# Kernel optimization log

Hardware: AMD Instinct MI355X
Metric: run time of the kernel (lower is better)

The kernel has to match this reference:

```python
import jax, jax.numpy as jnp
import numpy as np
import math

B = 1024
G = 34  # grid_dim = 17*2
C = 4
SCENT = 19


def _scent_kernel_np():
    h = w = SCENT
    mx, my = 0.5 * h, 0.5 * w
    sx, sy = h / 4.0, w / 4.0
    x = np.linspace(0.0, h, h)
    y = np.linspace(0.0, w, w)
    X, Y = np.meshgrid(x, y, indexing='ij')
    z = (1.0 / (2.0 * math.pi * sx * sy)) * np.exp(-(((X - mx) ** 2) / (2 * sx ** 2) + ((Y - my) ** 2) / (2 * sy ** 2)))
    return (z * 80.0).astype(np.float32)


def setup_inputs() -> dict:
    key = jax.random.key(0)
    k1, k2, k3, k4 = jax.random.split(key, 4)
    cell = jax.random.uniform(k1, (B, C, G, G), dtype=jnp.float32)
    food = (jax.random.uniform(k2, (B, G, G), dtype=jnp.float32) > 0.97).astype(jnp.float32)
    fc1_w = jax.random.normal(k3, (64, 12), dtype=jnp.float32) * (1.0 / np.sqrt(12))
    fc1_b = jnp.zeros((64,), dtype=jnp.float32)
    fc2_w = jax.random.normal(k4, (4, 64), dtype=jnp.float32) * (1.0 / np.sqrt(64))
    fc2_b = jnp.zeros((4,), dtype=jnp.float32)
    scent_kernel = jnp.asarray(_scent_kernel_np())
    return {"cell": cell, "food": food, "fc1_w": fc1_w, "fc1_b": fc1_b,
            "fc2_w": fc2_w, "fc2_b": fc2_b, "scent_kernel": scent_kernel, "steps": 32}


def _conv(x, w, pad, groups):
    # x: [B, Cin, H, W], w: [Cout, Cin/groups, kh, kw]; cross-correlation like torch
    return jax.lax.conv_general_dilated(
        x, w, window_strides=(1, 1), padding=[(pad, pad), (pad, pad)],
        feature_group_count=groups, dimension_numbers=('NCHW', 'OIHW', 'NCHW'))


def _maxpool3(x):
    # 3x3 max pool, stride 1, pad 1 (pad value -inf, matching torch MaxPool2d semantics)
    return jax.lax.reduce_window(x, -jnp.inf, jax.lax.max, (1, 1, 3, 3), (1, 1, 1, 1),
                                 [(0, 0), (0, 0), (1, 1), (1, 1)])


def _forward(cell, food, fc1_w, fc1_b, fc2_w, fc2_b, scent_kernel, steps):
    dx = jnp.outer(jnp.array([1., 2., 1.], jnp.float32), jnp.array([-1., 0., 1.], jnp.float32)) / 8.0
    dy = dx.T
    kdx = jnp.tile(dx[None, None], (4, 1, 1, 1))  # depthwise, groups=4
    kdy = jnp.tile(dy[None, None], (4, 1, 1, 1))

    # perceive_scent: 19x19 gaussian conv, padding 9
    scent = _conv(food[:, None], scent_kernel[None, None], 9, 1)[:, 0]  # [B,G,G]

    def step(cell, _):
        cell = cell.at[:, 3].set(scent)
        # current living count per batch (cells in channel 0 above 0.8)
        cl = jnp.sum((cell[:, 0] > 0.8).astype(jnp.float32), axis=(1, 2))
        pre_mask = _maxpool3(cell[:, 0:1]) > 0.1  # [B,1,G,G]
        # perception: x, sobel-x, sobel-y -> 12 channels
        y1 = _conv(cell, kdx, 1, 4)
        y2 = _conv(cell, kdy, 1, 4)
        y = jnp.concatenate([cell, y1, y2], axis=1)  # [B,12,G,G]
        # tiny MLP per pixel (torch transposes dims 1<->3; linear over channels is equivalent)
        h = jax.nn.relu(jnp.einsum('bchw,oc->bohw', y, fc1_w) + fc1_b[None, :, None, None])
        upd = jnp.einsum('bchw,oc->bohw', h, fc2_w) + fc2_b[None, :, None, None]
        x = cell + upd
        post_mask = _maxpool3(x[:, 0:1]) > 0.1
        x = x * (pre_mask & post_mask).astype(x.dtype)
        x = jnp.clip(x, -10.0, 10.0)
        x = x.at[:, 0].set(jnp.clip(x[:, 0], 0.0, 1.0))
        # keep_k_largest: threshold = cl-th smallest (ascending sort index == cl); keep strictly greater
        flat = x[:, 0].reshape(B, -1)  # [B, G*G]
        srt = jnp.sort(flat, axis=1)
        kth = jnp.take_along_axis(srt, cl.astype(jnp.int32)[:, None], axis=1)  # [B,1] (gather clamps OOB)
        flat = jnp.where(flat > kth, flat, 0.0)
        x = x.at[:, 0].set(flat.reshape(B, G, G))
        return x, None

    cell, _ = jax.lax.scan(jax.checkpoint(step), cell, None, length=steps)
    total_pixel_val = cell[:, 0:1].sum(axis=(1, 2, 3))
    living_count = jnp.sum((cell[:, 0:1] > 0.1).astype(jnp.float32), axis=(1, 2, 3))
    return cell, food, total_pixel_val, living_count


def reference(cell, food, fc1_w, fc1_b, fc2_w, fc2_b, scent_kernel, steps):
    return _forward(cell, food, fc1_w, fc1_b, fc2_w, fc2_b, scent_kernel, steps)
```

## Files before the change

kernel.cpp:

```cpp
#include <hip/hip_runtime.h>
#include <stdint.h>

#define GD    34
#define RS    39
#define NROW  36
#define CBN   (NROW*RS)
#define NPIX  1156
#define NT    256
#define NB    1024
#define TPR   7
#define TUSED 238
#define FS    57
#define SCRN  2960

#define SCAN_PASS(KK) do {                                                         \
    if (wid == 0) {                                                                \
      const int base2 = lane << 4;                                                 \
      int c16[16]; int csum = 0;                                                   \
      _Pragma("unroll")                                                            \
      for (int j = 0; j < 16; ++j) { c16[j] = hist[base2+j]; hist[base2+j] = 0; csum += c16[j]; } \
      int inc = csum;                                                              \
      _Pragma("unroll")                                                            \
      for (int off2 = 1; off2 < 64; off2 <<= 1) { int vv = __shfl_up(inc, off2); if (lane >= off2) inc += vv; } \
      const int excl = inc - csum;                                                 \
      if ((KK) >= excl && (KK) < inc) {                                            \
        int rem = (KK) - excl; int cum = 0;                                        \
        _Pragma("unroll")                                                          \
        for (int j = 0; j < 16; ++j) {                                             \
          if (rem >= cum && rem < cum + c16[j]) { sel_bin = base2 + j; sel_rem = rem - cum; } \
          cum += c16[j];                                                           \
        }                                                                          \
      }                                                                            \
    }                                                                              \
  } while (0)

__global__ __launch_bounds__(NT) __attribute__((amdgpu_waves_per_eu(4, 4)))
void ca_kernel(const float* __restrict__ cell_in,
               const float* __restrict__ food_in,
               const float* __restrict__ fc1_w,
               const float* __restrict__ fc1_b,
               const float* __restrict__ fc2_w,
               const float* __restrict__ fc2_b,
               const float* __restrict__ sk_g,
               const int*   __restrict__ steps_p,
               float* __restrict__ out)
{
  __shared__ float cbuf[3][CBN];
  __shared__ float scratch[SCRN];
  __shared__ int   icl[2][4];
  __shared__ int   inzaz[4];
  __shared__ int   sel_bin, sel_rem;
  __shared__ float fsum[4];
  __shared__ int   lcnt[4];

  float* x0buf = scratch;
  int*   premi = (int*)(scratch + 1404);
  int*   hist  = (int*)scratch;

  const int tid  = threadIdx.x;
  const int b    = blockIdx.x;
  const int lane = tid & 63;
  const int wid  = tid >> 6;
  const int nsteps = steps_p[0];

  const bool tval = (tid < TUSED);
  const int  trow = tval ? (tid / TPR) : 0;
  const int  c0   = tval ? ((tid % TPR) * 5) : 0;
  const int  nval = tval ? ((c0 <= 29) ? 5 : 4) : 0;
  const int  pb0  = tval ? ((trow+1)*RS + c0 + 1) : (RS+1);
  const int  p0   = trow*GD + c0;

  for (int idx = tid; idx < 3*CBN; idx += NT) (&cbuf[0][0])[idx] = 0.f;
  for (int idx = tid; idx < SCRN;  idx += NT) scratch[idx] = 0.f;
  __syncthreads();

  float v3k[5], v1k[5], v2k[5];
  int cnt0 = 0;
#pragma unroll
  for (int j = 0; j < 5; ++j) {
    v3k[j] = 0.f; v1k[j] = 0.f; v2k[j] = 0.f;
    if (j < nval) {
      int p = p0 + j;
      const float* gi = cell_in + (size_t)b*4*NPIX + p;
      float v0 = gi[0], v1 = gi[NPIX], v2 = gi[2*NPIX], v3 = gi[3*NPIX];
      cbuf[0][pb0+j] = v0; cbuf[1][pb0+j] = v1; cbuf[2][pb0+j] = v2;
      v3k[j] = v3;
      cnt0 += (v0 > 0.8f) ? 1 : 0;
      scratch[(trow+9)*FS + (c0+j+9)] = food_in[(size_t)b*NPIX + p];
    }
  }
#pragma unroll
  for (int off = 32; off; off >>= 1) cnt0 += __shfl_down(cnt0, off);
  if (lane == 0) icl[0][wid] = cnt0;
  __syncthreads();

  float scent[5] = {0.f, 0.f, 0.f, 0.f, 0.f};
  for (int dr = 0; dr < 19; ++dr) {
    const float* frow = scratch + (trow+dr)*FS + c0;
    float f[23];
#pragma unroll
    for (int q = 0; q < 23; ++q) f[q] = frow[q];
    const float* krow = sk_g + dr*19;
#pragma unroll
    for (int dc = 0; dc < 19; ++dc) {
      const float kv = krow[dc];
      scent[0] = fmaf(f[dc+0], kv, scent[0]);
      scent[1] = fmaf(f[dc+1], kv, scent[1]);
      scent[2] = fmaf(f[dc+2], kv, scent[2]);
      scent[3] = fmaf(f[dc+3], kv, scent[3]);
      scent[4] = fmaf(f[dc+4], kv, scent[4]);
    }
  }
  __syncthreads();
  for (int idx = tid; idx < SCRN; idx += NT) scratch[idx] = 0.f;
  __syncthreads();
#pragma unroll
  for (int j = 0; j < 5; ++j) if (j < nval) x0buf[pb0+j] = scent[j];
  __syncthreads();
  float sxs[5], sys[5];
#pragma unroll
  for (int j = 0; j < 5; ++j) {
    const int bb = (j < nval) ? (pb0 + j) : pb0;
    float t00=x0buf[bb-RS-1], t01=x0buf[bb-RS], t02=x0buf[bb-RS+1];
    float t10=x0buf[bb-1],                      t12=x0buf[bb+1];
    float t20=x0buf[bb+RS-1], t21=x0buf[bb+RS], t22=x0buf[bb+RS+1];
    sxs[j] = ((t02 - t00) + 2.f*(t12 - t10) + (t22 - t20)) * 0.125f;
    sys[j] = ((t20 - t00) + 2.f*(t21 - t01) + (t22 - t02)) * 0.125f;
  }

  const float b2r0 = fc2_b[0], b2r1 = fc2_b[1], b2r2 = fc2_b[2], b2r3 = fc2_b[3];

  for (int s = 0; s < nsteps; ++s) {
    __syncthreads();
    float r0[7], r1[7], r2[7], cm[7];
#pragma unroll
    for (int jc = 0; jc < 7; ++jc) {
      r0[jc] = 0.f; r1[jc] = 0.f; r2[jc] = 0.f; cm[jc] = 0.f;
      if (jc < nval + 2) {
        const int a = pb0 - 1 + jc;
        r0[jc] = cbuf[0][a-RS]; r1[jc] = cbuf[0][a]; r2[jc] = cbuf[0][a+RS];
        cm[jc] = fmaxf(fmaxf(r0[jc], r1[jc]), r2[jc]);
      }
    }
    unsigned pm = 0;
#pragma unroll
    for (int j = 0; j < 5; ++j) {
      if (j < nval) {
        bool t = fmaxf(fmaxf(cm[j], cm[j+1]), cm[j+2]) > 0.1f;
        premi[pb0+j] = t ? 1 : 0;
        if (t) pm |= (1u << j);
      }
    }
    __syncthreads();
    int co[7];
#pragma unroll
    for (int jc = 0; jc < 7; ++jc) {
      co[jc] = 0;
      if (jc < nval + 2) {
        const int a = pb0 - 1 + jc;
        co[jc] = premi[a-RS] | premi[a] | premi[a+RS];
      }
    }
#pragma unroll
    for (int j = 0; j < 5; ++j) {
      int acti = (j < nval) ? (co[j] | co[j+1] | co[j+2]) : 0;
      if (__any(acti)) {
        const int bb = pb0 + j;
        float y0,y1,y2,y4,y5,y6,y8,y9,y10;
        {
          y0 = r1[j+1];
          y4 = ((r0[j+2] - r0[j]) + 2.f*(r1[j+2] - r1[j]) + (r2[j+2] - r2[j])) * 0.125f;
          y8 = ((r2[j] - r0[j]) + 2.f*(r2[j+1] - r0[j+1]) + (r2[j+2] - r0[j+2])) * 0.125f;
        }
        {
          const float* cb = cbuf[1];
          float t00=cb[bb-RS-1], t01=cb[bb-RS], t02=cb[bb-RS+1];
          float t10=cb[bb-1],    t11=cb[bb],    t12=cb[bb+1];
          float t20=cb[bb+RS-1], t21=cb[bb+RS], t22=cb[bb+RS+1];
          y1 = t11;
          y5 = ((t02 - t00) + 2.f*(t12 - t10) + (t22 - t20)) * 0.125f;
          y9 = ((t20 - t00) + 2.f*(t21 - t01) + (t22 - t02)) * 0.125f;
        }
        {
          const float* cb = cbuf[2];
          float t00=cb[bb-RS-1], t01=cb[bb-RS], t02=cb[bb-RS+1];
          float t10=cb[bb-1],    t11=cb[bb],    t12=cb[bb+1];
          float t20=cb[bb+RS-1], t21=cb[bb+RS], t22=cb[bb+RS+1];
          y2 = t11;
          y6 = ((t02 - t00) + 2.f*(t12 - t10) + (t22 - t20)) * 0.125f;
          y10= ((t20 - t00) + 2.f*(t21 - t01) + (t22 - t02)) * 0.125f;
        }
        const float y3 = scent[j], y7 = sxs[j], y11 = sys[j];
        float u0 = b2r0, u1 = b2r1, u2 = b2r2, u3 = b2r3;
        for (int o = 0; o < 64; ++o) {
          const float* wr = fc1_w + o*12;
          float t = fc1_b[o];
          t = fmaf(y0, wr[0], t);  t = fmaf(y1, wr[1], t);
          t = fmaf(y2, wr[2], t);  t = fmaf(y3, wr[3], t);
          t = fmaf(y4, wr[4], t);  t = fmaf(y5, wr[5], t);
          t = fmaf(y6, wr[6], t);  t = fmaf(y7, wr[7], t);
          t = fmaf(y8, wr[8], t);  t = fmaf(y9, wr[9], t);
          t = fmaf(y10, wr[10], t); t = fmaf(y11, wr[11], t);
          t = fmaxf(t, 0.f);
          u0 = fmaf(t, fc2_w[o],     u0);
          u1 = fmaf(t, fc2_w[64+o],  u1);
          u2 = fmaf(t, fc2_w[128+o], u2);
          u3 = fmaf(t, fc2_w[192+o], u3);
        }
        v3k[j] = y3 + u3;
        if (j < nval) {
          x0buf[bb]  = y0 + u0;
          v1k[j]     = y1 + u1;
          v2k[j]     = y2 + u2;
        }
      }
    }
    __syncthreads();
    unsigned pq = 0;
    float midv[5];
#pragma unroll
    for (int j = 0; j < 5; ++j) midv[j] = 0.f;
    if (pm) {
      float dm[7];
#pragma unroll
      for (int jc = 0; jc < 7; ++jc) {
        dm[jc] = 0.f;
        if (jc < nval + 2) {
          const int a = pb0 - 1 + jc;
          float u = x0buf[a-RS], m = x0buf[a], d = x0buf[a+RS];
          dm[jc] = fmaxf(fmaxf(u, m), d);
          if (jc >= 1 && jc <= 5) midv[jc-1] = m;
        }
      }
#pragma unroll
      for (int j = 0; j < 5; ++j)
        if (fmaxf(fmaxf(dm[j], dm[j+1]), dm[j+2]) > 0.1f) pq |= (1u << j);
    }
    int packed = 0;
    float v0s[5];
#pragma unroll
    for (int j = 0; j < 5; ++j) {
      v0s[j] = 0.f;
      if (j < nval) {
        bool alive = ((pm >> j) & 1u) && ((pq >> j) & 1u);
        float v0 = 0.f, v1 = 0.f, v2 = 0.f, v3 = 0.f;
        if (alive) {
          v0 = fminf(fmaxf(midv[j],   0.f),  1.f);
          v1 = fminf(fmaxf(v1k[j],  -10.f), 10.f);
          v2 = fminf(fmaxf(v2k[j],  -10.f), 10.f);
          v3 = fminf(fmaxf(v3k[j],  -10.f), 10.f);
        }
        cbuf[1][pb0+j] = v1; cbuf[2][pb0+j] = v2; v3k[j] = v3;
        v0s[j] = v0;
        int zer = (v0 == 0.f) ? 1 : 0;
        int azf = (zer && v1 == 0.f && v2 == 0.f && v3 == 0.f) ? 1 : 0;
        packed += zer + (azf << 16);
      }
    }
#pragma unroll
    for (int off = 32; off; off >>= 1) packed += __shfl_down(packed, off);
    if (lane == 0) inzaz[wid] = packed;
    __syncthreads();
    const int t01 = inzaz[0]+inzaz[1]+inzaz[2]+inzaz[3];
    const int nz = t01 & 0xffff, az = t01 >> 16;
    const int cl = icl[s&1][0]+icl[s&1][1]+icl[s&1][2]+icl[s&1][3];
    const int k  = (cl < NPIX) ? cl : (NPIX-1);
    float kth = 0.f;
    if (k >= nz) {
      hist[tid] = 0; hist[tid+256] = 0; hist[tid+512] = 0; hist[tid+768] = 0;
      __syncthreads();
      const int k2 = k - nz;
#pragma unroll
      for (int j = 0; j < 5; ++j) {
        unsigned u = __float_as_uint(v0s[j]);
        if (j < nval && u != 0u) atomicAdd(&hist[u >> 20], 1);
      }
      __syncthreads();
      SCAN_PASS(k2);
      __syncthreads();
      const int bin1 = sel_bin; const int kr2 = sel_rem;
#pragma unroll
      for (int j = 0; j < 5; ++j) {
        unsigned u = __float_as_uint(v0s[j]);
        if (j < nval && u != 0u && (u >> 20) == (unsigned)bin1)
          atomicAdd(&hist[(u >> 10) & 1023u], 1);
      }
      __syncthreads();
      SCAN_PASS(kr2);
      __syncthreads();
      const int bin2 = sel_bin; const int kr3 = sel_rem;
      const unsigned pref2 = (((unsigned)bin1) << 10) | (unsigned)bin2;
#pragma unroll
      for (int j = 0; j < 5; ++j) {
        unsigned u = __float_as_uint(v0s[j]);
        if (j < nval && u != 0u && (u >> 10) == pref2)
          atomicAdd(&hist[u & 1023u], 1);
      }
      __syncthreads();
      SCAN_PASS(kr3);
      __syncthreads();
      kth = __uint_as_float((((unsigned)bin1) << 20) | (((unsigned)bin2) << 10) | (unsigned)sel_bin);
    }
    int cnt = 0;
#pragma unroll
    for (int j = 0; j < 5; ++j) {
      if (j < nval) {
        float w0 = (v0s[j] > kth) ? v0s[j] : 0.f;
        cbuf[0][pb0+j] = w0;
        cnt += (w0 > 0.8f) ? 1 : 0;
      }
    }
#pragma unroll
    for (int off = 32; off; off >>= 1) cnt += __shfl_down(cnt, off);
    if (lane == 0) icl[(s+1)&1][wid] = cnt;
    if (az == NPIX) break;
  }

  const size_t CELL_N = (size_t)4*NPIX*NB;
  const size_t FOOD_N = (size_t)NPIX*NB;
  float tp = 0.f; int lcv = 0;
#pragma unroll
  for (int j = 0; j < 5; ++j) {
    if (j < nval) {
      const int p = p0 + j;
      float c0v = cbuf[0][pb0+j], c1 = cbuf[1][pb0+j], c2 = cbuf[2][pb0+j];
      size_t go = (size_t)b*4*NPIX + p;
      out[go]          = c0v;
      out[go +   NPIX] = c1;
      out[go + 2*NPIX] = c2;
      out[go + 3*NPIX] = v3k[j];
      out[CELL_N + (size_t)b*NPIX + p] = food_in[(size_t)b*NPIX + p];
      tp += c0v;
      lcv += (c0v > 0.1f) ? 1 : 0;
    }
  }
#pragma unroll
  for (int off = 32; off; off >>= 1) { tp += __shfl_down(tp, off); lcv += __shfl_down(lcv, off); }
  if (lane == 0) { fsum[wid] = tp; lcnt[wid] = lcv; }
  __syncthreads();
  if (tid == 0) {
    out[CELL_N + FOOD_N + b]      = fsum[0]+fsum[1]+fsum[2]+fsum[3];
    out[CELL_N + FOOD_N + NB + b] = (float)(lcnt[0]+lcnt[1]+lcnt[2]+lcnt[3]);
  }
}

extern "C" void kernel_launch(void* const* d_in, const int* in_sizes, int n_in,
                              void* d_out, int out_size, void* d_ws, size_t ws_size,
                              hipStream_t stream) {
  const float* cell  = (const float*)d_in[0];
  const float* food  = (const float*)d_in[1];
  const float* fc1w  = (const float*)d_in[2];
  const float* fc1b  = (const float*)d_in[3];
  const float* fc2w  = (const float*)d_in[4];
  const float* fc2b  = (const float*)d_in[5];
  const float* sk    = (const float*)d_in[6];
  const int*   steps = (const int*)d_in[7];
  float* out = (float*)d_out;
  ca_kernel<<<NB, NT, 0, stream>>>(cell, food, fc1w, fc1b, fc2w, fc2b, sk, steps, out);
}
```

Before: 236.9 us.

## Compute activity mask from 5x5 max window, dropping premask shared buffer and barrier

Channel 0 now lives in a buffer with a two-pixel halo, so each thread can derive the dilated pre-mask (activity) directly from a 5x5 max window held in registers. This removes the premask write to shared memory, one __syncthreads per step, and the reloads of neighbour flags. The Sobel loads are also batched into register row windows, with compute gated once per wavefront instead of per pixel. In exchange each thread does more shared loads and max operations and holds more registers, which could hurt occupancy under the fixed waves-per-EU setting.

```diff
diff --git a/kernel.cpp b/kernel.cpp
--- a/kernel.cpp
+++ b/kernel.cpp
@@ -3,8 +3,8 @@
 
 #define GD    34
 #define RS    39
-#define NROW  36
-#define CBN   (NROW*RS)
+#define C0N   (38*RS)
+#define CBN   (36*RS)
 #define NPIX  1156
 #define NT    256
 #define NB    1024
@@ -45,7 +45,9 @@
                const int*   __restrict__ steps_p,
                float* __restrict__ out)
 {
-  __shared__ float cbuf[3][CBN];
+  __shared__ float c0b[C0N];
+  __shared__ float cbuf1[CBN];
+  __shared__ float cbuf2[CBN];
   __shared__ float scratch[SCRN];
   __shared__ int   icl[2][4];
   __shared__ int   inzaz[4];
@@ -54,7 +56,6 @@
   __shared__ int   lcnt[4];
 
   float* x0buf = scratch;
-  int*   premi = (int*)(scratch + 1404);
   int*   hist  = (int*)scratch;
 
   const int tid  = threadIdx.x;
@@ -67,11 +68,16 @@
   const int  trow = tval ? (tid / TPR) : 0;
   const int  c0   = tval ? ((tid % TPR) * 5) : 0;
   const int  nval = tval ? ((c0 <= 29) ? 5 : 4) : 0;
-  const int  pb0  = tval ? ((trow+1)*RS + c0 + 1) : (RS+1);
+  const int  pb0c = (trow+2)*RS + c0 + 2;
+  const int  pb1  = (trow+1)*RS + c0 + 1;
   const int  p0   = trow*GD + c0;
-
-  for (int idx = tid; idx < 3*CBN; idx += NT) (&cbuf[0][0])[idx] = 0.f;
-  for (int idx = tid; idx < SCRN;  idx += NT) scratch[idx] = 0.f;
+  const int  wb0  = trow*RS + c0;
+  const int  wb1  = trow*RS + c0;
+
+  for (int idx = tid; idx < C0N;  idx += NT) c0b[idx]   = 0.f;
+  for (int idx = tid; idx < CBN;  idx += NT) cbuf1[idx] = 0.f;
+  for (int idx = tid; idx < CBN;  idx += NT) cbuf2[idx] = 0.f;
+  for (int idx = tid; idx < SCRN; idx += NT) scratch[idx] = 0.f;
   __syncthreads();
 
   float v3k[5], v1k[5], v2k[5];
@@ -83,7 +89,7 @@
       int p = p0 + j;
       const float* gi = cell_in + (size_t)b*4*NPIX + p;
       float v0 = gi[0], v1 = gi[NPIX], v2 = gi[2*NPIX], v3 = gi[3*NPIX];
-      cbuf[0][pb0+j] = v0; cbuf[1][pb0+j] = v1; cbuf[2][pb0+j] = v2;
+      c0b[pb0c+j] = v0; cbuf1[pb1+j] = v1; cbuf2[pb1+j] = v2;
       v3k[j] = v3;
       cnt0 += (v0 > 0.8f) ? 1 : 0;
       scratch[(trow+9)*FS + (c0+j+9)] = food_in[(size_t)b*NPIX + p];
@@ -115,12 +121,12 @@
   for (int idx = tid; idx < SCRN; idx += NT) scratch[idx] = 0.f;
   __syncthreads();
 #pragma unroll
-  for (int j = 0; j < 5; ++j) if (j < nval) x0buf[pb0+j] = scent[j];
+  for (int j = 0; j < 5; ++j) if (j < nval) x0buf[pb1+j] = scent[j];
   __syncthreads();
   float sxs[5], sys[5];
 #pragma unroll
   for (int j = 0; j < 5; ++j) {
-    const int bb = (j < nval) ? (pb0 + j) : pb0;
+    const int bb = (j < nval) ? (pb1 + j) : pb1;
     float t00=x0buf[bb-RS-1], t01=x0buf[bb-RS], t02=x0buf[bb-RS+1];
     float t10=x0buf[bb-1],                      t12=x0buf[bb+1];
     float t20=x0buf[bb+RS-1], t21=x0buf[bb+RS], t22=x0buf[bb+RS+1];
@@ -132,86 +138,97 @@
 
   for (int s = 0; s < nsteps; ++s) {
     __syncthreads();
-    float r0[7], r1[7], r2[7], cm[7];
-#pragma unroll
-    for (int jc = 0; jc < 7; ++jc) {
-      r0[jc] = 0.f; r1[jc] = 0.f; r2[jc] = 0.f; cm[jc] = 0.f;
-      if (jc < nval + 2) {
-        const int a = pb0 - 1 + jc;
-        r0[jc] = cbuf[0][a-RS]; r1[jc] = cbuf[0][a]; r2[jc] = cbuf[0][a+RS];
-        cm[jc] = fmaxf(fmaxf(r0[jc], r1[jc]), r2[jc]);
-      }
-    }
-    unsigned pm = 0;
+    float a0[9], a4[9], m3[9], r0[9], r1[9], r2[9];
+#pragma unroll
+    for (int q = 0; q < 9; ++q) a0[q] = c0b[wb0 + q];
+#pragma unroll
+    for (int q = 0; q < 9; ++q) { r0[q] = c0b[wb0 + RS + q];   m3[q] = r0[q]; }
+#pragma unroll
+    for (int q = 0; q < 9; ++q) { r1[q] = c0b[wb0 + 2*RS + q]; m3[q] = fmaxf(m3[q], r1[q]); }
+#pragma unroll
+    for (int q = 0; q < 9; ++q) { r2[q] = c0b[wb0 + 3*RS + q]; m3[q] = fmaxf(m3[q], r2[q]); }
+#pragma unroll
+    for (int q = 0; q < 9; ++q) a4[q] = c0b[wb0 + 4*RS + q];
+    float m5[9];
+#pragma unroll
+    for (int q = 0; q < 9; ++q) m5[q] = fmaxf(fmaxf(a0[q], m3[q]), a4[q]);
+    unsigned pm = 0, am = 0;
 #pragma unroll
     for (int j = 0; j < 5; ++j) {
       if (j < nval) {
-        bool t = fmaxf(fmaxf(cm[j], cm[j+1]), cm[j+2]) > 0.1f;
-        premi[pb0+j] = t ? 1 : 0;
-        if (t) pm |= (1u << j);
-      }
-    }
-    __syncthreads();
-    int co[7];
-#pragma unroll
-    for (int jc = 0; jc < 7; ++jc) {
-      co[jc] = 0;
-      if (jc < nval + 2) {
-        const int a = pb0 - 1 + jc;
-        co[jc] = premi[a-RS] | premi[a] | premi[a+RS];
-      }
-    }
+        if (fmaxf(fmaxf(m3[j+1], m3[j+2]), m3[j+3]) > 0.1f) pm |= (1u << j);
+        float mm5 = fmaxf(fmaxf(fmaxf(fmaxf(m5[j], m5[j+1]), m5[j+2]), m5[j+3]), m5[j+4]);
+        if (mm5 > 0.1f) am |= (1u << j);
+      }
+    }
+    float y0a[5], y4a[5], y8a[5];
 #pragma unroll
     for (int j = 0; j < 5; ++j) {
-      int acti = (j < nval) ? (co[j] | co[j+1] | co[j+2]) : 0;
-      if (__any(acti)) {
-        const int bb = pb0 + j;
-        float y0,y1,y2,y4,y5,y6,y8,y9,y10;
-        {
-          y0 = r1[j+1];
-          y4 = ((r0[j+2] - r0[j]) + 2.f*(r1[j+2] - r1[j]) + (r2[j+2] - r2[j])) * 0.125f;
-          y8 = ((r2[j] - r0[j]) + 2.f*(r2[j+1] - r0[j+1]) + (r2[j+2] - r0[j+2])) * 0.125f;
-        }
-        {
-          const float* cb = cbuf[1];
-          float t00=cb[bb-RS-1], t01=cb[bb-RS], t02=cb[bb-RS+1];
-          float t10=cb[bb-1],    t11=cb[bb],    t12=cb[bb+1];
-          float t20=cb[bb+RS-1], t21=cb[bb+RS], t22=cb[bb+RS+1];
-          y1 = t11;
-          y5 = ((t02 - t00) + 2.f*(t12 - t10) + (t22 - t20)) * 0.125f;
-          y9 = ((t20 - t00) + 2.f*(t21 - t01) + (t22 - t02)) * 0.125f;
-        }
-        {
-          const float* cb = cbuf[2];
-          float t00=cb[bb-RS-1], t01=cb[bb-RS], t02=cb[bb-RS+1];
-          float t10=cb[bb-1],    t11=cb[bb],    t12=cb[bb+1];
-          float t20=cb[bb+RS-1], t21=cb[bb+RS], t22=cb[bb+RS+1];
-          y2 = t11;
-          y6 = ((t02 - t00) + 2.f*(t12 - t10) + (t22 - t20)) * 0.125f;
-          y10= ((t20 - t00) + 2.f*(t21 - t01) + (t22 - t02)) * 0.125f;
-        }
-        const float y3 = scent[j], y7 = sxs[j], y11 = sys[j];
-        float u0 = b2r0, u1 = b2r1, u2 = b2r2, u3 = b2r3;
-        for (int o = 0; o < 64; ++o) {
-          const float* wr = fc1_w + o*12;
-          float t = fc1_b[o];
-          t = fmaf(y0, wr[0], t);  t = fmaf(y1, wr[1], t);
-          t = fmaf(y2, wr[2], t);  t = fmaf(y3, wr[3], t);
-          t = fmaf(y4, wr[4], t);  t = fmaf(y5, wr[5], t);
-          t = fmaf(y6, wr[6], t);  t = fmaf(y7, wr[7], t);
-          t = fmaf(y8, wr[8], t);  t = fmaf(y9, wr[9], t);
-          t = fmaf(y10, wr[10], t); t = fmaf(y11, wr[11], t);
-          t = fmaxf(t, 0.f);
-          u0 = fmaf(t, fc2_w[o],     u0);
-          u1 = fmaf(t, fc2_w[64+o],  u1);
-          u2 = fmaf(t, fc2_w[128+o], u2);
-          u3 = fmaf(t, fc2_w[192+o], u3);
-        }
-        v3k[j] = y3 + u3;
-        if (j < nval) {
-          x0buf[bb]  = y0 + u0;
-          v1k[j]     = y1 + u1;
-          v2k[j]     = y2 + u2;
+      y0a[j] = r1[j+2];
+      y4a[j] = ((r0[j+3] - r0[j+1]) + 2.f*(r1[j+3] - r1[j+1]) + (r2[j+3] - r2[j+1])) * 0.125f;
+      y8a[j] = ((r2[j+1] - r0[j+1]) + 2.f*(r2[j+2] - r0[j+2]) + (r2[j+3] - r0[j+3])) * 0.125f;
+    }
+    if (__any(am != 0u)) {
+      float y1a[5], y5a[5], y9a[5], y2a[5], y6a[5], y10a[5];
+      {
+        float s0[7], s1[7], s2[7];
+#pragma unroll
+        for (int q = 0; q < 7; ++q) s0[q] = cbuf1[wb1 + q];
+#pragma unroll
+        for (int q = 0; q < 7; ++q) s1[q] = cbuf1[wb1 + RS + q];
+#pragma unroll
+        for (int q = 0; q < 7; ++q) s2[q] = cbuf1[wb1 + 2*RS + q];
+#pragma unroll
+        for (int j = 0; j < 5; ++j) {
+          y1a[j] = s1[j+1];
+          y5a[j] = ((s0[j+2] - s0[j]) + 2.f*(s1[j+2] - s1[j]) + (s2[j+2] - s2[j])) * 0.125f;
+          y9a[j] = ((s2[j]   - s0[j]) + 2.f*(s2[j+1] - s0[j+1]) + (s2[j+2] - s0[j+2])) * 0.125f;
+        }
+      }
+      {
+        float s0[7], s1[7], s2[7];
+#pragma unroll
+        for (int q = 0; q < 7; ++q) s0[q] = cbuf2[wb1 + q];
+#pragma unroll
+        for (int q = 0; q < 7; ++q) s1[q] = cbuf2[wb1 + RS + q];
+#pragma unroll
+        for (int q = 0; q < 7; ++q) s2[q] = cbuf2[wb1 + 2*RS + q];
+#pragma unroll
+        for (int j = 0; j < 5; ++j) {
+          y2a[j]  = s1[j+1];
+          y6a[j]  = ((s0[j+2] - s0[j]) + 2.f*(s1[j+2] - s1[j]) + (s2[j+2] - s2[j])) * 0.125f;
+          y10a[j] = ((s2[j]   - s0[j]) + 2.f*(s2[j+1] - s0[j+1]) + (s2[j+2] - s0[j+2])) * 0.125f;
+        }
+      }
+#pragma unroll
+      for (int j = 0; j < 5; ++j) {
+        int acti = (j < nval) ? (int)((am >> j) & 1u) : 0;
+        if (__any(acti)) {
+          const float y0 = y0a[j], y1 = y1a[j], y2 = y2a[j],  y3  = scent[j];
+          const float y4 = y4a[j], y5 = y5a[j], y6 = y6a[j],  y7  = sxs[j];
+          const float y8 = y8a[j], y9 = y9a[j], y10 = y10a[j], y11 = sys[j];
+          float u0 = b2r0, u1 = b2r1, u2 = b2r2, u3 = b2r3;
+          for (int o = 0; o < 64; ++o) {
+            const float* wr = fc1_w + o*12;
+            float t = fc1_b[o];
+            t = fmaf(y0, wr[0], t);  t = fmaf(y1, wr[1], t);
+            t = fmaf(y2, wr[2], t);  t = fmaf(y3, wr[3], t);
+            t = fmaf(y4, wr[4], t);  t = fmaf(y5, wr[5], t);
+            t = fmaf(y6, wr[6], t);  t = fmaf(y7, wr[7], t);
+            t = fmaf(y8, wr[8], t);  t = fmaf(y9, wr[9], t);
+            t = fmaf(y10, wr[10], t); t = fmaf(y11, wr[11], t);
+            t = fmaxf(t, 0.f);
+            u0 = fmaf(t, fc2_w[o],     u0);
+            u1 = fmaf(t, fc2_w[64+o],  u1);
+            u2 = fmaf(t, fc2_w[128+o], u2);
+            u3 = fmaf(t, fc2_w[192+o], u3);
+          }
+          v3k[j] = y3 + u3;
+          if (j < nval) {
+            x0buf[pb1+j] = y0 + u0;
+            v1k[j]       = y1 + u1;
+            v2k[j]       = y2 + u2;
+          }
         }
       }
     }
@@ -226,7 +243,7 @@
       for (int jc = 0; jc < 7; ++jc) {
         dm[jc] = 0.f;
         if (jc < nval + 2) {
-          const int a = pb0 - 1 + jc;
+          const int a = pb1 - 1 + jc;
           float u = x0buf[a-RS], m = x0buf[a], d = x0buf[a+RS];
           dm[jc] = fmaxf(fmaxf(u, m), d);
           if (jc >= 1 && jc <= 5) midv[jc-1] = m;
@@ -250,7 +267,7 @@
           v2 = fminf(fmaxf(v2k[j],  -10.f), 10.f);
           v3 = fminf(fmaxf(v3k[j],  -10.f), 10.f);
         }
-        cbuf[1][pb0+j] = v1; cbuf[2][pb0+j] = v2; v3k[j] = v3;
+        cbuf1[pb1+j] = v1; cbuf2[pb1+j] = v2; v3k[j] = v3;
         v0s[j] = v0;
         int zer = (v0 == 0.f) ? 1 : 0;
         int azf = (zer && v1 == 0.f && v2 == 0.f && v3 == 0.f) ? 1 : 0;
@@ -306,7 +323,7 @@
     for (int j = 0; j < 5; ++j) {
       if (j < nval) {
         float w0 = (v0s[j] > kth) ? v0s[j] : 0.f;
-        cbuf[0][pb0+j] = w0;
+        c0b[pb0c+j] = w0;
         cnt += (w0 > 0.8f) ? 1 : 0;
       }
     }
@@ -323,7 +340,7 @@
   for (int j = 0; j < 5; ++j) {
     if (j < nval) {
       const int p = p0 + j;
-      float c0v = cbuf[0][pb0+j], c1 = cbuf[1][pb0+j], c2 = cbuf[2][pb0+j];
+      float c0v = c0b[pb0c+j], c1 = cbuf1[pb1+j], c2 = cbuf2[pb1+j];
       size_t go = (size_t)b*4*NPIX + p;
       out[go]          = c0v;
       out[go +   NPIX] = c1;
```

Measured after the change: 239.0 us. Within noise of the previous version (+0.9%).
